# Kernel tuning notes

Hardware: AMD Instinct MI355X
Metric: run time of the kernel (lower is better)

The kernel has to match this reference:

```python
import jax, jax.numpy as jnp
import numpy as np

# --- MLA config (matches init_kwargs) ---
DIM = 2048
H = 16
KV_RANK = 512
Q_RANK = 1536
ROPE = 64          # qk_rope_head_dim (even)
NOPE = 128         # qk_nope_head_dim
VD = 128           # v_head_dim
THETA = 500000.0
EPS = 1e-6
B, T = 1, 2048
QK_HEAD = NOPE + ROPE  # logits use nope + rope dims


def _rmsnorm(x, w):
    # x float32; RMS over last dim, no mean subtraction
    rms = jax.lax.rsqrt(jnp.mean(x * x, axis=-1, keepdims=True) + EPS)
    return (x * rms) * w


def _rope_tables(t):
    inv_freq = 1.0 / (THETA ** (jnp.arange(0, ROPE, 2, dtype=jnp.float32) / ROPE))  # (ROPE/2,)
    pos = jnp.arange(t, dtype=jnp.float32)
    angles = jnp.outer(pos, inv_freq)  # (T, ROPE/2)
    return jnp.cos(angles), jnp.sin(angles)


def _apply_rope(x, cos, sin):
    # x: (B, T, Hx, D) with adjacent-pair rotation; cos/sin: (T, D/2)
    b, t, h, d = x.shape
    xp = x.reshape(b, t, h, d // 2, 2)
    even, odd = xp[..., 0], xp[..., 1]
    c = cos.reshape(1, t, 1, d // 2)
    s = sin.reshape(1, t, 1, d // 2)
    out = jnp.stack((even * c - odd * s, odd * c + even * s), axis=-1)
    return out.reshape(b, t, h, d)


def setup_inputs() -> dict:
    key = jax.random.key(0)
    ks = jax.random.split(key, 7)
    s = 0.02
    x = jax.random.normal(ks[0], (B, T, DIM), dtype=jnp.float32)
    w_q_down = jax.random.normal(ks[1], (Q_RANK, DIM), dtype=jnp.float32) * s
    q_norm_w = jnp.ones((Q_RANK,), dtype=jnp.float32)
    w_q_up = jax.random.normal(ks[2], (H * (NOPE + ROPE), Q_RANK), dtype=jnp.float32) * s
    w_kv_down = jax.random.normal(ks[3], (KV_RANK + ROPE, DIM), dtype=jnp.float32) * s
    kv_norm_w = jnp.ones((KV_RANK,), dtype=jnp.float32)
    w_kv_up = jax.random.normal(ks[4], (H * (NOPE + VD), KV_RANK), dtype=jnp.float32) * s
    w_o = jax.random.normal(ks[5], (DIM, H * VD), dtype=jnp.float32) * s
    return {"x": x, "w_q_down": w_q_down, "q_norm_w": q_norm_w, "w_q_up": w_q_up,
            "w_kv_down": w_kv_down, "kv_norm_w": kv_norm_w, "w_kv_up": w_kv_up, "w_o": w_o}


def reference(x, w_q_down, q_norm_w, w_q_up, w_kv_down, kv_norm_w, w_kv_up, w_o):
    b, t, _ = x.shape
    # Query path: down-proj -> RMSNorm -> up-proj, split nope/rope
    c_q = _rmsnorm(x @ w_q_down.T, q_norm_w)                       # (B,T,Q_RANK)
    q = (c_q @ w_q_up.T).reshape(b, t, H, NOPE + ROPE)
    q_nope, q_rope = q[..., :NOPE], q[..., NOPE:]
    # KV path: down-proj -> split latent c_kv and shared rope key
    kv = x @ w_kv_down.T                                           # (B,T,KV_RANK+ROPE)
    c_kv = kv[..., :KV_RANK]
    k_rope_raw = kv[..., KV_RANK:].reshape(b, t, 1, ROPE)
    # RoPE (adjacent-pair), start_pos=0
    cos, sin = _rope_tables(t)
    q_rope = _apply_rope(q_rope, cos, sin)
    k_rope = _apply_rope(k_rope_raw, cos, sin)                     # (B,T,1,ROPE) shared head
    # Reconstruct k_nope and v from normalized latent
    kv_up = (_rmsnorm(c_kv, kv_norm_w) @ w_kv_up.T).reshape(b, t, H, NOPE + VD)
    k_nope, v = kv_up[..., :NOPE], kv_up[..., NOPE:]
    # Assemble full q/k (rope key broadcast across heads)
    q_full = jnp.concatenate((q_nope, q_rope), axis=-1)            # (B,T,H,QK_HEAD)
    k_full = jnp.concatenate((k_nope, jnp.broadcast_to(k_rope, (b, t, H, ROPE))), axis=-1)
    # Causal attention
    scale = 1.0 / np.sqrt(QK_HEAD)
    scores = jnp.einsum('bqhd,bkhd->bhqk', q_full, k_full) * scale  # (B,H,T,T)
    causal = jnp.tril(jnp.ones((t, t), dtype=bool))
    scores = jnp.where(causal[None, None], scores, -jnp.inf)
    attn = jax.nn.softmax(scores, axis=-1)
    out = jnp.einsum('bhqk,bkhd->bqhd', attn, v).reshape(b, t, H * VD)
    return out @ w_o.T                                             # (B,T,DIM)
```

## Files before the change

### kernel.cpp

```cpp
#include <hip/hip_runtime.h>
#include <hip/hip_bf16.h>

typedef short short8 __attribute__((ext_vector_type(8)));
typedef float f32x4 __attribute__((ext_vector_type(4)));

#define DIM 2048
#define NH 16
#define KV_RANK 512
#define Q_RANK 1536
#define ROPE_D 64
#define NOPE 128
#define VD 128
#define TT 2048
#define QKH 192
#define QD (NH * QKH)
#define KVUP_D (NH * (NOPE + VD))
#define WDN 2176

__device__ inline unsigned short f2bf(float f) {
  __hip_bfloat16 h = __float2bfloat16(f);
  union { __hip_bfloat16 h; unsigned short u; } cv; cv.h = h; return cv.u;
}
__device__ inline float bf2f(unsigned short u) {
  union { unsigned int i; float f; } cv; cv.i = ((unsigned int)u) << 16; return cv.f;
}
__device__ inline void gload_lds16(const void* g, void* l) {
  __builtin_amdgcn_global_load_lds(
      (const __attribute__((address_space(1))) void*)g,
      (__attribute__((address_space(3))) void*)l, 16, 0, 0);
}

__global__ __launch_bounds__(256) void convert_all(
    const float* __restrict__ x, const float* __restrict__ wqd,
    const float* __restrict__ wkvd, const float* __restrict__ wqu,
    const float* __restrict__ wkvu, const float* __restrict__ wo,
    unsigned short* __restrict__ xb, unsigned short* __restrict__ wdb,
    unsigned short* __restrict__ wqub, unsigned short* __restrict__ wkvub,
    unsigned short* __restrict__ wob) {
  int i = blockIdx.x * 256 + threadIdx.x;
  const int n0 = TT * DIM / 4;
  const int n1 = WDN * 2048 / 4;
  const int n2 = QD * Q_RANK / 4;
  const int n3 = KVUP_D * KV_RANK / 4;
  const int n4 = DIM * DIM / 4;
  float4 v;
  unsigned short* dst;
  if (i < n0) { v = reinterpret_cast<const float4*>(x)[i]; dst = xb; }
  else if ((i -= n0) < n1) {
    int row = i >> 9, c4 = i & 511;
    if (row < 1536)      v = reinterpret_cast<const float4*>(wqd)[row * 512 + c4];
    else if (row < 2112) v = reinterpret_cast<const float4*>(wkvd)[(row - 1536) * 512 + c4];
    else                 v = make_float4(0.f, 0.f, 0.f, 0.f);
    dst = wdb;
  }
  else if ((i -= n1) < n2) { v = reinterpret_cast<const float4*>(wqu)[i]; dst = wqub; }
  else if ((i -= n2) < n3) { v = reinterpret_cast<const float4*>(wkvu)[i]; dst = wkvub; }
  else if ((i -= n3) < n4) { v = reinterpret_cast<const float4*>(wo)[i]; dst = wob; }
  else return;
  ushort4 o;
  o.x = f2bf(v.x); o.y = f2bf(v.y); o.z = f2bf(v.z); o.w = f2bf(v.w);
  reinterpret_cast<ushort4*>(dst)[i] = o;
}

__device__ __forceinline__ void gemm_core(const unsigned short* __restrict__ A,
                                          const unsigned short* __restrict__ W,
                                          unsigned short* As, unsigned short* Bs,
                                          int K, int lda, int ldb,
                                          int bm, int bn, int tid,
                                          f32x4 (&acc)[4][4]) {
  const int lane = tid & 63, wave = tid >> 6;
  const int wm = (wave >> 1) * 64, wn = (wave & 1) * 64;
  const int fr = lane & 15, fg = lane >> 4;
  const int sr = lane >> 3, scb = (lane & 7) ^ sr;
  const int r0 = wave * 32;

  const unsigned short* Ag = A + (size_t)(bm + r0 + sr) * lda + scb * 8;
  const unsigned short* Wg = W + (size_t)(bn + r0 + sr) * ldb + scb * 8;
  const int nt = K >> 6;

#pragma unroll
  for (int i = 0; i < 4; ++i) {
    gload_lds16(Ag + (size_t)(i * 8) * lda, As + r0 * 64 + i * 512);
    gload_lds16(Wg + (size_t)(i * 8) * ldb, Bs + r0 * 64 + i * 512);
  }
  int cur = 0;
  for (int t = 0; t < nt; ++t) {
    if (t + 1 < nt) {
      const int nb = cur ^ 1;
      const int ko = (t + 1) * 64;
#pragma unroll
      for (int i = 0; i < 4; ++i) {
        gload_lds16(Ag + ko + (size_t)(i * 8) * lda, As + nb * 8192 + r0 * 64 + i * 512);
        gload_lds16(Wg + ko + (size_t)(i * 8) * ldb, Bs + nb * 8192 + r0 * 64 + i * 512);
      }
      asm volatile("s_waitcnt vmcnt(8)" ::: "memory");
    } else {
      asm volatile("s_waitcnt vmcnt(0)" ::: "memory");
    }
    __builtin_amdgcn_s_barrier();
    asm volatile("" ::: "memory");
    const unsigned short* Ac = As + cur * 8192;
    const unsigned short* Bc = Bs + cur * 8192;
    __builtin_amdgcn_s_setprio(1);
#pragma unroll
    for (int kk = 0; kk < 2; ++kk) {
      short8 a[4], b[4];
#pragma unroll
      for (int i = 0; i < 4; ++i) {
        int ra = wm + i * 16 + fr;
        a[i] = *reinterpret_cast<const short8*>(&Ac[ra * 64 + (((kk * 4 + fg) ^ (ra & 7)) * 8)]);
        int rb = wn + i * 16 + fr;
        b[i] = *reinterpret_cast<const short8*>(&Bc[rb * 64 + (((kk * 4 + fg) ^ (rb & 7)) * 8)]);
      }
#pragma unroll
      for (int i = 0; i < 4; ++i)
#pragma unroll
        for (int j = 0; j < 4; ++j)
          acc[i][j] = __builtin_amdgcn_mfma_f32_16x16x32_bf16(a[i], b[j], acc[i][j], 0, 0, 0);
    }
    __builtin_amdgcn_s_setprio(0);
    asm volatile("" ::: "memory");
    __builtin_amdgcn_s_barrier();
    cur ^= 1;
  }
}

__global__ __launch_bounds__(256) void gemm_fast(const unsigned short* __restrict__ A,
                                                 const unsigned short* __restrict__ W,
                                                 float* __restrict__ Cf,
                                                 unsigned short* __restrict__ Cb,
                                                 int K, int lda, int ldb, int ldc) {
  __shared__ __align__(16) unsigned short As[2 * 128 * 64];
  __shared__ __align__(16) unsigned short Bs[2 * 128 * 64];
  const int tid = threadIdx.x;
  const int w = blockIdx.y * gridDim.x + blockIdx.x;
  const int nwg = gridDim.x * gridDim.y;
  const int s = (w & 7) * (nwg >> 3) + (w >> 3);
  const int bxs = s % gridDim.x, bys = s / gridDim.x;
  const int bm = bys * 128, bn = bxs * 128;
  const int lane = tid & 63, wave = tid >> 6;
  const int wm = (wave >> 1) * 64, wn = (wave & 1) * 64;
  const int fr = lane & 15, fg = lane >> 4;

  f32x4 acc[4][4] = {};
  gemm_core(A, W, As, Bs, K, lda, ldb, bm, bn, tid, acc);

  if (Cb) {
#pragma unroll
    for (int i = 0; i < 4; ++i) {
      int row0 = bm + wm + i * 16 + fg * 4;
#pragma unroll
      for (int j = 0; j < 4; ++j) {
        int col = bn + wn + j * 16 + fr;
#pragma unroll
        for (int r = 0; r < 4; ++r)
          Cb[(size_t)(row0 + r) * ldc + col] = f2bf(acc[i][j][r]);
      }
    }
  } else {
#pragma unroll
    for (int i = 0; i < 4; ++i) {
      int row0 = bm + wm + i * 16 + fg * 4;
#pragma unroll
      for (int j = 0; j < 4; ++j) {
        int col = bn + wn + j * 16 + fr;
#pragma unroll
        for (int r = 0; r < 4; ++r)
          Cf[(size_t)(row0 + r) * ldc + col] = acc[i][j][r];
      }
    }
  }
}

__global__ __launch_bounds__(256) void gemm_dual(
    const unsigned short* __restrict__ A1, const unsigned short* __restrict__ W1,
    unsigned short* __restrict__ C1,
    const unsigned short* __restrict__ A2, const unsigned short* __restrict__ W2,
    unsigned short* __restrict__ kbuf, unsigned short* __restrict__ vt) {
  __shared__ __align__(16) unsigned short As[2 * 128 * 64];
  __shared__ __align__(16) unsigned short Bs[2 * 128 * 64];
  const int tid = threadIdx.x;
  const int w = blockIdx.x;
  const int nwg = gridDim.x;
  const int s = (w & 7) * (nwg >> 3) + (w >> 3);
  const unsigned short *A, *W;
  int K, lda, bm, bn;
  const bool isq = (s < 384);
  if (isq) {
    A = A1; W = W1; K = Q_RANK; lda = Q_RANK;
    bn = (s % 24) * 128; bm = (s / 24) * 128;
  } else {
    int b2 = s - 384;
    A = A2; W = W2; K = KV_RANK; lda = KV_RANK;
    bn = (b2 & 31) * 128; bm = (b2 >> 5) * 128;
  }
  const int lane = tid & 63, wave = tid >> 6;
  const int wm = (wave >> 1) * 64, wn = (wave & 1) * 64;
  const int fr = lane & 15, fg = lane >> 4;

  f32x4 acc[4][4] = {};
  gemm_core(A, W, As, Bs, K, lda, lda, bm, bn, tid, acc);

  if (isq) {
#pragma unroll
    for (int i = 0; i < 4; ++i) {
      int row0 = bm + wm + i * 16 + fg * 4;
#pragma unroll
      for (int j = 0; j < 4; ++j) {
        int col = bn + wn + j * 16 + fr;
#pragma unroll
        for (int r = 0; r < 4; ++r)
          C1[(size_t)(row0 + r) * QD + col] = f2bf(acc[i][j][r]);
      }
    }
  } else {
#pragma unroll
    for (int i = 0; i < 4; ++i) {
      int row0 = bm + wm + i * 16 + fg * 4;
#pragma unroll
      for (int j = 0; j < 4; ++j) {
        int col = bn + wn + j * 16 + fr;
        int hh = col >> 8, cc = col & 255;
        if (cc < 128) {
#pragma unroll
          for (int r = 0; r < 4; ++r)
            kbuf[((size_t)hh * TT + row0 + r) * QKH + cc] = f2bf(acc[i][j][r]);
        } else {
          ushort4 w4;
          w4.x = f2bf(acc[i][j][0]); w4.y = f2bf(acc[i][j][1]);
          w4.z = f2bf(acc[i][j][2]); w4.w = f2bf(acc[i][j][3]);
          *reinterpret_cast<ushort4*>(vt + (size_t)(hh * VD + cc - 128) * TT + row0) = w4;
        }
      }
    }
  }
}

__global__ __launch_bounds__(256) void rmsnorm_both(
    const unsigned short* __restrict__ cqkv,
    const float* __restrict__ qw, const float* __restrict__ kvw,
    unsigned short* __restrict__ cq, unsigned short* __restrict__ ckv) {
  const int row = blockIdx.x, tid = threadIdx.x;
  __shared__ float red[256];
  const unsigned short* base = cqkv + (size_t)row * WDN;

#pragma unroll
  for (int ph = 0; ph < 2; ++ph) {
    const int cols = ph ? KV_RANK : Q_RANK;
    const int nch = cols >> 3;
    const unsigned short* x = base + (ph ? Q_RANK : 0);
    const float* w = ph ? kvw : qw;
    unsigned short* out = (ph ? ckv : cq) + (size_t)row * cols;
    float ss = 0.f;
    for (int cb = tid; cb < nch; cb += 256) {
      short8 v = *reinterpret_cast<const short8*>(x + cb * 8);
#pragma unroll
      for (int e = 0; e < 8; ++e) { float f = bf2f((unsigned short)v[e]); ss += f * f; }
    }
    red[tid] = ss; __syncthreads();
    for (int off = 128; off > 0; off >>= 1) {
      if (tid < off) red[tid] += red[tid + off];
      __syncthreads();
    }
    float r = rsqrtf(red[0] / (float)cols + 1e-6f);
    __syncthreads();
    for (int cb = tid; cb < nch; cb += 256) {
      short8 v = *reinterpret_cast<const short8*>(x + cb * 8);
      ushort4 o0, o1;
      o0.x = f2bf(bf2f((unsigned short)v[0]) * r * w[cb * 8 + 0]);
      o0.y = f2bf(bf2f((unsigned short)v[1]) * r * w[cb * 8 + 1]);
      o0.z = f2bf(bf2f((unsigned short)v[2]) * r * w[cb * 8 + 2]);
      o0.w = f2bf(bf2f((unsigned short)v[3]) * r * w[cb * 8 + 3]);
      o1.x = f2bf(bf2f((unsigned short)v[4]) * r * w[cb * 8 + 4]);
      o1.y = f2bf(bf2f((unsigned short)v[5]) * r * w[cb * 8 + 5]);
      o1.z = f2bf(bf2f((unsigned short)v[6]) * r * w[cb * 8 + 6]);
      o1.w = f2bf(bf2f((unsigned short)v[7]) * r * w[cb * 8 + 7]);
      *reinterpret_cast<ushort4*>(out + cb * 8) = o0;
      *reinterpret_cast<ushort4*>(out + cb * 8 + 4) = o1;
    }
  }
}

__global__ __launch_bounds__(256) void rope_kernel(unsigned short* __restrict__ qb,
                                                   const unsigned short* __restrict__ cqkv,
                                                   unsigned short* __restrict__ kbuf) {
  const int t = blockIdx.x, tid = threadIdx.x;
  unsigned short* qrow = qb + (size_t)t * QD;
  for (int p = tid; p < NH * 32 + 32; p += 256) {
    int j = (p < NH * 32) ? (p & 31) : (p - NH * 32);
    float inv = powf(500000.0f, -(float)(2 * j) * (1.0f / 64.0f));
    float ang = (float)t * inv;
    float sv, cv;
    sincosf(ang, &sv, &cv);
    if (p < NH * 32) {
      int h = p >> 5;
      unsigned short* b = qrow + h * QKH + NOPE + 2 * j;
      float e = bf2f(b[0]), o = bf2f(b[1]);
      b[0] = f2bf(e * cv - o * sv);
      b[1] = f2bf(o * cv + e * sv);
    } else {
      const unsigned short* b = cqkv + (size_t)t * WDN + 2048 + 2 * j;
      float e = bf2f(b[0]), o = bf2f(b[1]);
      unsigned short re = f2bf(e * cv - o * sv);
      unsigned short ro = f2bf(o * cv + e * sv);
#pragma unroll
      for (int hh = 0; hh < NH; ++hh) {
        kbuf[((size_t)hh * TT + t) * QKH + NOPE + 2 * j]     = re;
        kbuf[((size_t)hh * TT + t) * QKH + NOPE + 2 * j + 1] = ro;
      }
    }
  }
}

__global__ __launch_bounds__(256, 2) void attn_part(
    const unsigned short* __restrict__ qb,
    const unsigned short* __restrict__ kbuf,
    const unsigned short* __restrict__ vtb,
    unsigned short* __restrict__ Opart,
    float* __restrict__ ml)
{
  const int b = blockIdx.x;
  const int h = b & 15;
  const int w = b >> 4;
  int qt, c;
  if (w < 16)      { qt = 15 - (w >> 2); c = w & 3; }
  else if (w < 28) { int v = w - 16; qt = 11 - v / 3; c = v % 3; }
  else if (w < 36) { qt = 7 - ((w - 28) >> 1); c = (w - 28) & 1; }
  else             { qt = 3 - (w - 36); c = 0; }
  const int t0 = qt * 128;
  const int ktlo = c * 8;
  const int kthi = min(c * 8 + 8, 2 * qt + 2);
  const int tid = threadIdx.x;
  const int lane = tid & 63, wv = tid >> 6;
  const int fr = lane & 15, fg = lane >> 4;

  __shared__ __align__(16) unsigned short KVl[2560 * 8];
  __shared__ __align__(16) unsigned short Ps[4][2][16 * 64];
  unsigned short* Kl = KVl;
  unsigned short* Vt = KVl + 12288;

  short8 qf[2][6];
#pragma unroll
  for (int s = 0; s < 2; ++s) {
    const unsigned short* qrow = qb + (size_t)(t0 + wv * 32 + s * 16 + fr) * QD + h * QKH;
#pragma unroll
    for (int kc = 0; kc < 6; ++kc)
      qf[s][kc] = *reinterpret_cast<const short8*>(qrow + kc * 32 + fg * 8);
  }

  f32x4 o[2][8] = {};
  float m2[2] = {-1e30f, -1e30f};
  float l2[2] = {0.f, 0.f};
  const float scale = 0.0721687836487032f;
  const unsigned short* kb = kbuf + (size_t)h * TT * QKH;
  const unsigned short* vb = vtb + (size_t)h * VD * TT;

  for (int kt = ktlo; kt < kthi; ++kt) {
    const int kt0 = kt * 64;
#pragma unroll
    for (int i = 0; i < 6; ++i) {
      int u = tid + i * 256;
      int row = u / 24, cb = u - (u / 24) * 24;
      int cbs = cb ^ (row & 7);
      gload_lds16(kb + (size_t)(kt0 + row) * QKH + cbs * 8, Kl + u * 8);
    }
#pragma unroll
    for (int i = 0; i < 4; ++i) {
      int u = tid + i * 256;
      int d = u >> 3, cb = u & 7;
      int cbs = cb ^ (d & 7);
      gload_lds16(vb + (size_t)d * TT + kt0 + cbs * 8, Vt + u * 8);
    }
    asm volatile("s_waitcnt vmcnt(0)" ::: "memory");
    __syncthreads();

    f32x4 sA[2][4] = {};
    __builtin_amdgcn_s_setprio(1);
#pragma unroll
    for (int kc = 0; kc < 6; ++kc) {
#pragma unroll
      for (int kr = 0; kr < 4; ++kr) {
        int row = kr * 16 + fr;
        short8 kf = *reinterpret_cast<const short8*>(
            &Kl[row * QKH + (((kc * 4 + fg) ^ (row & 7)) * 8)]);
        sA[0][kr] = __builtin_amdgcn_mfma_f32_16x16x32_bf16(kf, qf[0][kc], sA[0][kr], 0, 0, 0);
        sA[1][kr] = __builtin_amdgcn_mfma_f32_16x16x32_bf16(kf, qf[1][kc], sA[1][kr], 0, 0, 0);
      }
    }
    __builtin_amdgcn_s_setprio(0);

    const bool diag = (kt0 + 64 > t0);
#pragma unroll
    for (int s = 0; s < 2; ++s) {
      const int qg = t0 + wv * 32 + s * 16 + fr;
      float mx = -1e30f;
#pragma unroll
      for (int kr = 0; kr < 4; ++kr)
#pragma unroll
        for (int r = 0; r < 4; ++r) {
          float svv = sA[s][kr][r] * scale;
          if (diag && (kt0 + kr * 16 + fg * 4 + r) > qg) svv = -1e30f;
          sA[s][kr][r] = svv;
          mx = fmaxf(mx, svv);
        }
      mx = fmaxf(mx, __shfl_xor(mx, 16));
      mx = fmaxf(mx, __shfl_xor(mx, 32));
      float mn = fmaxf(m2[s], mx);
      float corr = __expf(m2[s] - mn);
      m2[s] = mn;
      float ssum = 0.f;
#pragma unroll
      for (int kr = 0; kr < 4; ++kr) {
        ushort4 pk;
        float p0 = __expf(sA[s][kr][0] - mn);
        float p1 = __expf(sA[s][kr][1] - mn);
        float p2 = __expf(sA[s][kr][2] - mn);
        float p3 = __expf(sA[s][kr][3] - mn);
        ssum += p0 + p1 + p2 + p3;
        pk.x = f2bf(p0); pk.y = f2bf(p1); pk.z = f2bf(p2); pk.w = f2bf(p3);
        *reinterpret_cast<ushort4*>(
            &Ps[wv][s][fr * 64 + (((kr * 2 + (fg >> 1)) ^ (fr & 7)) * 8) + (fg & 1) * 4]) = pk;
      }
      ssum += __shfl_xor(ssum, 16);
      ssum += __shfl_xor(ssum, 32);
      l2[s] = l2[s] * corr + ssum;
      if (__any(corr != 1.0f)) {
        float c0 = __shfl(corr, fg * 4 + 0);
        float c1 = __shfl(corr, fg * 4 + 1);
        float c2 = __shfl(corr, fg * 4 + 2);
        float c3 = __shfl(corr, fg * 4 + 3);
#pragma unroll
        for (int dj = 0; dj < 8; ++dj) {
          o[s][dj][0] *= c0; o[s][dj][1] *= c1;
          o[s][dj][2] *= c2; o[s][dj][3] *= c3;
        }
      }
    }

    __builtin_amdgcn_s_setprio(1);
#pragma unroll
    for (int kk = 0; kk < 2; ++kk) {
      short8 pa0 = *reinterpret_cast<const short8*>(
          &Ps[wv][0][fr * 64 + (((kk * 4 + fg) ^ (fr & 7)) * 8)]);
      short8 pa1 = *reinterpret_cast<const short8*>(
          &Ps[wv][1][fr * 64 + (((kk * 4 + fg) ^ (fr & 7)) * 8)]);
#pragma unroll
      for (int dj = 0; dj < 8; ++dj) {
        int dv = dj * 16 + fr;
        short8 bv = *reinterpret_cast<const short8*>(
            &Vt[dv * 64 + (((kk * 4 + fg) ^ (dv & 7)) * 8)]);
        o[0][dj] = __builtin_amdgcn_mfma_f32_16x16x32_bf16(pa0, bv, o[0][dj], 0, 0, 0);
        o[1][dj] = __builtin_amdgcn_mfma_f32_16x16x32_bf16(pa1, bv, o[1][dj], 0, 0, 0);
      }
    }
    __builtin_amdgcn_s_setprio(0);
    __syncthreads();
  }

  const int slot = (h * 16 + qt) * 4 + c;
#pragma unroll
  for (int s = 0; s < 2; ++s) {
#pragma unroll
    for (int r = 0; r < 4; ++r) {
      int row = wv * 32 + s * 16 + fg * 4 + r;
      unsigned short* orow = Opart + ((size_t)slot * 128 + row) * 128;
#pragma unroll
      for (int dj = 0; dj < 8; ++dj)
        orow[dj * 16 + fr] = f2bf(o[s][dj][r]);
    }
    if (fg == 0) {
      int row = wv * 32 + s * 16 + fr;
      ml[((size_t)slot * 128 + row) * 2]     = m2[s];
      ml[((size_t)slot * 128 + row) * 2 + 1] = l2[s];
    }
  }
}

__global__ __launch_bounds__(256) void attn_combine(
    const unsigned short* __restrict__ Opart, const float* __restrict__ ml,
    unsigned short* __restrict__ out) {
  const int bid = blockIdx.x;
  const int h = bid >> 5;
  const int qt = (bid >> 1) & 15;
  const int rh = bid & 1;
  const int nch = qt / 4 + 1;
  const int tid = threadIdx.x;
  const int row = rh * 64 + (tid >> 2), dg = tid & 3;
  const int base = (h * 16 + qt) * 4;
  float mm[4], ll[4];
  float M = -1e30f;
#pragma unroll
  for (int cc = 0; cc < 4; ++cc) {
    if (cc < nch) {
      mm[cc] = ml[((size_t)(base + cc) * 128 + row) * 2];
      ll[cc] = ml[((size_t)(base + cc) * 128 + row) * 2 + 1];
      M = fmaxf(M, mm[cc]);
    } else { mm[cc] = -1e30f; ll[cc] = 0.f; }
  }
  float L = 0.f;
#pragma unroll
  for (int cc = 0; cc < 4; ++cc) {
    mm[cc] = __expf(mm[cc] - M);
    L += ll[cc] * mm[cc];
  }
  float acc[32] = {};
#pragma unroll
  for (int cc = 0; cc < 4; ++cc) {
    if (cc < nch) {
      const unsigned short* op = Opart + ((size_t)(base + cc) * 128 + row) * 128 + dg * 32;
      float sc = mm[cc];
#pragma unroll
      for (int e8 = 0; e8 < 4; ++e8) {
        short8 v = *reinterpret_cast<const short8*>(op + e8 * 8);
#pragma unroll
        for (int e = 0; e < 8; ++e) acc[e8 * 8 + e] += bf2f((unsigned short)v[e]) * sc;
      }
    }
  }
  float linv = 1.0f / L;
  unsigned short* dst = out + (size_t)(qt * 128 + row) * DIM + h * VD + dg * 32;
#pragma unroll
  for (int e4 = 0; e4 < 8; ++e4) {
    ushort4 w4;
    w4.x = f2bf(acc[e4 * 4 + 0] * linv);
    w4.y = f2bf(acc[e4 * 4 + 1] * linv);
    w4.z = f2bf(acc[e4 * 4 + 2] * linv);
    w4.w = f2bf(acc[e4 * 4 + 3] * linv);
    *reinterpret_cast<ushort4*>(dst + e4 * 4) = w4;
  }
}

extern "C" void kernel_launch(void* const* d_in, const int* in_sizes, int n_in,
                              void* d_out, int out_size, void* d_ws, size_t ws_size,
                              hipStream_t stream) {
  const float* x        = (const float*)d_in[0];
  const float* w_q_down = (const float*)d_in[1];
  const float* q_norm_w = (const float*)d_in[2];
  const float* w_q_up   = (const float*)d_in[3];
  const float* w_kv_down= (const float*)d_in[4];
  const float* kv_norm_w= (const float*)d_in[5];
  const float* w_kv_up  = (const float*)d_in[6];
  const float* w_o      = (const float*)d_in[7];
  float* outp = (float*)d_out;

  char* ws = (char*)d_ws;
  size_t off = 0;
  auto alloc = [&](size_t bytes) {
    void* p = ws + off;
    off += (bytes + 255) & ~(size_t)255;
    return p;
  };
  unsigned short* x_bf     = (unsigned short*)alloc((size_t)TT * DIM * 2);
  unsigned short* wdown_bf = (unsigned short*)alloc((size_t)WDN * DIM * 2);
  unsigned short* wqu_bf   = (unsigned short*)alloc((size_t)QD * Q_RANK * 2);
  unsigned short* wkvu_bf  = (unsigned short*)alloc((size_t)KVUP_D * KV_RANK * 2);
  unsigned short* wo_bf    = (unsigned short*)alloc((size_t)DIM * DIM * 2);
  unsigned short* cqkv_bf  = (unsigned short*)alloc((size_t)TT * WDN * 2);
  unsigned short* cq_bf    = (unsigned short*)alloc((size_t)TT * Q_RANK * 2);
  unsigned short* ckv_bf   = (unsigned short*)alloc((size_t)TT * KV_RANK * 2);
  unsigned short* qb_bf    = (unsigned short*)alloc((size_t)TT * QD * 2);
  unsigned short* kbuf     = (unsigned short*)alloc((size_t)NH * TT * QKH * 2);
  unsigned short* vtb      = (unsigned short*)alloc((size_t)NH * VD * TT * 2);
  unsigned short* Opart    = (unsigned short*)alloc((size_t)1024 * 128 * 128 * 2);
  float*          mlbuf    = (float*)alloc((size_t)1024 * 128 * 2 * 4);
  unsigned short* attn_bf  = x_bf;

  {
    int total = TT * DIM / 4 + WDN * 2048 / 4 + QD * Q_RANK / 4 +
                KVUP_D * KV_RANK / 4 + DIM * DIM / 4;
    convert_all<<<dim3((total + 255) / 256), dim3(256), 0, stream>>>(
        x, w_q_down, w_kv_down, w_q_up, w_kv_up, w_o,
        x_bf, wdown_bf, wqu_bf, wkvu_bf, wo_bf);
  }

  dim3 blk(256);
  gemm_fast<<<dim3(WDN / 128, TT / 128), blk, 0, stream>>>(
      x_bf, wdown_bf, nullptr, cqkv_bf, DIM, DIM, DIM, WDN);
  rmsnorm_both<<<dim3(TT), blk, 0, stream>>>(cqkv_bf, q_norm_w, kv_norm_w, cq_bf, ckv_bf);
  gemm_dual<<<dim3(896), blk, 0, stream>>>(cq_bf, wqu_bf, qb_bf,
                                           ckv_bf, wkvu_bf, kbuf, vtb);
  rope_kernel<<<dim3(TT), blk, 0, stream>>>(qb_bf, cqkv_bf, kbuf);
  attn_part<<<dim3(640), blk, 0, stream>>>(qb_bf, kbuf, vtb, Opart, mlbuf);
  attn_combine<<<dim3(512), blk, 0, stream>>>(Opart, mlbuf, attn_bf);
  gemm_fast<<<dim3(DIM / 128, TT / 128), blk, 0, stream>>>(
      attn_bf, wo_bf, outp, nullptr, DIM, DIM, DIM, DIM);
}
```

Measured before the change: 229.2 us.

## Use single-buffered LDS GEMM core in dual GEMM and drop XCD block swizzle

Adds a single-buffered variant of the GEMM main loop that loads each K tile into LDS, synchronizes, computes, and synchronizes again, and uses it in the fused q/kv up-projection kernel. Shared memory per block drops by half, which may let more workgroups share a CU, but load latency is no longer overlapped with the MFMA work inside a block. It also removes the block-index remapping that spread consecutive tiles across XCDs in both GEMM kernels, so tiles are now assigned in plain launch order. That gives up the L2 locality the remapping was meant to provide.

```diff
diff --git a/kernel.cpp b/kernel.cpp
--- a/kernel.cpp
+++ b/kernel.cpp
@@ -125,6 +125,50 @@
   }
 }
 
+__device__ __forceinline__ void gemm_core_sb(const unsigned short* __restrict__ A,
+                                             const unsigned short* __restrict__ W,
+                                             unsigned short* As, unsigned short* Bs,
+                                             int K, int lda, int ldb,
+                                             int bm, int bn, int tid,
+                                             f32x4 (&acc)[4][4]) {
+  const int lane = tid & 63, wave = tid >> 6;
+  const int wm = (wave >> 1) * 64, wn = (wave & 1) * 64;
+  const int fr = lane & 15, fg = lane >> 4;
+  const int sr = lane >> 3, scb = (lane & 7) ^ sr;
+  const int r0 = wave * 32;
+
+  const unsigned short* Ag = A + (size_t)(bm + r0 + sr) * lda + scb * 8;
+  const unsigned short* Wg = W + (size_t)(bn + r0 + sr) * ldb + scb * 8;
+
+  for (int k0 = 0; k0 < K; k0 += 64) {
+#pragma unroll
+    for (int i = 0; i < 4; ++i) {
+      gload_lds16(Ag + k0 + (size_t)(i * 8) * lda, As + r0 * 64 + i * 512);
+      gload_lds16(Wg + k0 + (size_t)(i * 8) * ldb, Bs + r0 * 64 + i * 512);
+    }
+    __syncthreads();
+    __builtin_amdgcn_s_setprio(1);
+#pragma unroll
+    for (int kk = 0; kk < 2; ++kk) {
+      short8 a[4], b[4];
+#pragma unroll
+      for (int i = 0; i < 4; ++i) {
+        int ra = wm + i * 16 + fr;
+        a[i] = *reinterpret_cast<const short8*>(&As[ra * 64 + (((kk * 4 + fg) ^ (ra & 7)) * 8)]);
+        int rb = wn + i * 16 + fr;
+        b[i] = *reinterpret_cast<const short8*>(&Bs[rb * 64 + (((kk * 4 + fg) ^ (rb & 7)) * 8)]);
+      }
+#pragma unroll
+      for (int i = 0; i < 4; ++i)
+#pragma unroll
+        for (int j = 0; j < 4; ++j)
+          acc[i][j] = __builtin_amdgcn_mfma_f32_16x16x32_bf16(a[i], b[j], acc[i][j], 0, 0, 0);
+    }
+    __builtin_amdgcn_s_setprio(0);
+    __syncthreads();
+  }
+}
+
 __global__ __launch_bounds__(256) void gemm_fast(const unsigned short* __restrict__ A,
                                                  const unsigned short* __restrict__ W,
                                                  float* __restrict__ Cf,
@@ -133,11 +177,7 @@
   __shared__ __align__(16) unsigned short As[2 * 128 * 64];
   __shared__ __align__(16) unsigned short Bs[2 * 128 * 64];
   const int tid = threadIdx.x;
-  const int w = blockIdx.y * gridDim.x + blockIdx.x;
-  const int nwg = gridDim.x * gridDim.y;
-  const int s = (w & 7) * (nwg >> 3) + (w >> 3);
-  const int bxs = s % gridDim.x, bys = s / gridDim.x;
-  const int bm = bys * 128, bn = bxs * 128;
+  const int bm = blockIdx.y * 128, bn = blockIdx.x * 128;
   const int lane = tid & 63, wave = tid >> 6;
   const int wm = (wave >> 1) * 64, wn = (wave & 1) * 64;
   const int fr = lane & 15, fg = lane >> 4;
@@ -177,12 +217,10 @@
     unsigned short* __restrict__ C1,
     const unsigned short* __restrict__ A2, const unsigned short* __restrict__ W2,
     unsigned short* __restrict__ kbuf, unsigned short* __restrict__ vt) {
-  __shared__ __align__(16) unsigned short As[2 * 128 * 64];
-  __shared__ __align__(16) unsigned short Bs[2 * 128 * 64];
+  __shared__ __align__(16) unsigned short As[128 * 64];
+  __shared__ __align__(16) unsigned short Bs[128 * 64];
   const int tid = threadIdx.x;
-  const int w = blockIdx.x;
-  const int nwg = gridDim.x;
-  const int s = (w & 7) * (nwg >> 3) + (w >> 3);
+  const int s = blockIdx.x;
   const unsigned short *A, *W;
   int K, lda, bm, bn;
   const bool isq = (s < 384);
@@ -199,7 +237,7 @@
   const int fr = lane & 15, fg = lane >> 4;
 
   f32x4 acc[4][4] = {};
-  gemm_core(A, W, As, Bs, K, lda, lda, bm, bn, tid, acc);
+  gemm_core_sb(A, W, As, Bs, K, lda, lda, bm, bn, tid, acc);
 
   if (isq) {
 #pragma unroll
```

Measured after the change: 213.1 us. 1.08x faster.
